# Kernel tuning notes

Measured on AMD Instinct MI355X. Metric: run time of the kernel, lower is better.

The kernel has to match this reference:

```python
import jax, jax.numpy as jnp
import numpy as np

OMEGA = 30.0
N_PTS, D_IN, HID, D_OUT, N_BLOCKS = 262144, 3, 128, 1, 7


def setup_inputs() -> dict:
    key = jax.random.key(0)
    ks = jax.random.split(key, 10)
    u = lambda k, shape, lim: jax.random.uniform(k, shape, jnp.float32, -lim, lim)
    # SIREN-style coordinates in [-1, 1]
    x = jax.random.uniform(ks[0], (N_PTS, D_IN), jnp.float32, -1.0, 1.0)
    # first SineLayer: uniform(-1/in, 1/in)
    W0 = u(ks[1], (HID, D_IN), 1.0 / D_IN)
    b0 = u(ks[2], (HID,), 1.0 / np.sqrt(D_IN))
    # hidden sine layers: uniform(-sqrt(6/in)/omega, sqrt(6/in)/omega)
    lim = np.sqrt(6.0 / HID) / OMEGA
    Wa = u(ks[3], (N_BLOCKS, HID, HID), lim)
    ba = u(ks[4], (N_BLOCKS, HID), 1.0 / np.sqrt(HID))
    Wb = u(ks[5], (N_BLOCKS, HID, HID), lim)
    bb = u(ks[6], (N_BLOCKS, HID), 1.0 / np.sqrt(HID))
    # final linear: uniform(-sqrt(6/in)/30, sqrt(6/in)/30)
    Wf = u(ks[7], (D_OUT, HID), np.sqrt(6.0 / HID) / 30.0)
    bf = u(ks[8], (D_OUT,), 1.0 / np.sqrt(HID))
    return {"x": x, "W0": W0, "b0": b0, "Wa": Wa, "ba": ba,
            "Wb": Wb, "bb": bb, "Wf": Wf, "bf": bf}


def reference(x, W0, b0, Wa, ba, Wb, bb, Wf, bf):
    # First SineLayer: sin(omega * (x W0^T + b0))   -> [N, HID]
    h = jnp.sin(OMEGA * (x @ W0.T + b0))
    nb = Wa.shape[0]
    # weight_1 = 0.5 when ave_first (ndx > 1, i.e. all blocks after the first)
    w1 = jnp.where(jnp.arange(nb) > 0, 0.5, 1.0).astype(h.dtype)
    # weight_2 = 0.5 when ave_second (last residual block)
    w2 = jnp.where(jnp.arange(nb) == nb - 1, 0.5, 1.0).astype(h.dtype)

    def block(h, xs):
        Wa_i, ba_i, Wb_i, bb_i, w1_i, w2_i = xs
        s1 = jnp.sin(OMEGA * ((w1_i * h) @ Wa_i.T + ba_i))
        s2 = jnp.sin(OMEGA * (s1 @ Wb_i.T + bb_i))
        return w2_i * (h + s2), None

    h, _ = jax.lax.scan(block, h, (Wa, ba, Wb, bb, w1, w2))
    return h @ Wf.T + bf  # [N, 1]
```

## Files before the change

kernel.cpp:

```cpp
#include <hip/hip_runtime.h>

#define NPTS 262144
#define HID  128
#define NB   7
#define NMAT 14

typedef __attribute__((ext_vector_type(8))) short bf16x8;
typedef __attribute__((ext_vector_type(4))) float f32x4;
typedef __attribute__((ext_vector_type(4))) unsigned int u32x4;

constexpr float OMEGA  = 30.0f;
constexpr float INV2PI = 0.15915494309189535f;

#define WIMG_BYTES (NMAT*32768)
#define BIAS_ELEMS (NMAT*128)
__device__ __align__(16) unsigned char g_img[WIMG_BYTES + BIAS_ELEMS*4];

__device__ __forceinline__ unsigned short f2bf(float v) {
    unsigned int u = __float_as_uint(v);
    u += 0x7fffu + ((u >> 16) & 1u);
    return (unsigned short)(u >> 16);
}

__device__ __forceinline__ float sin_rev(float r) {
    return __builtin_amdgcn_sinf(__builtin_amdgcn_fractf(r));
}

__device__ __forceinline__ unsigned int cvtpk(float lo, float hi) {
    unsigned int r;
    asm("v_cvt_pk_bf16_f32 %0, %1, %2" : "=v"(r) : "v"(lo), "v"(hi));
    return r;
}

__global__ void prep(const float* __restrict__ Wa, const float* __restrict__ ba,
                     const float* __restrict__ Wb, const float* __restrict__ bb) {
    int idx = blockIdx.x * 256 + threadIdx.x;
    const float bscale = OMEGA * INV2PI;
    const int total = NMAT * HID * HID;
    if (idx < total) {
        int mi = idx >> 14, rc = idx & 16383;
        int row = rc >> 7, col = rc & 127;
        int l = mi >> 1;
        float sc = bscale, v;
        if (mi & 1) v = Wb[l*16384 + rc];
        else { v = Wa[l*16384 + rc]; if (l > 0) sc *= 0.5f; }
        int t = col >> 4, g = (col >> 2) & 3, r = col & 3;
        int kp = ((t >> 1) << 5) | (g << 3) | ((t & 1) << 2) | r;
        int byte = mi*32768 + row*256 + ((kp*2) ^ ((row & 7) << 4));
        *(unsigned short*)(g_img + byte) = f2bf(v * sc);
    } else if (idx < total + BIAS_ELEMS) {
        int e = idx - total;
        int j = e >> 7, f = e & 127, l = j >> 1;
        float v = (j & 1) ? bb[l*HID + f] : ba[l*HID + f];
        ((float*)(g_img + WIMG_BYTES))[e] = v * bscale;
    }
}

#define LDS_BYTES 72704

__launch_bounds__(512, 2)
__global__ void siren_mlp(const float* __restrict__ x,
                          const float* __restrict__ W0,
                          const float* __restrict__ b0,
                          const float* __restrict__ Wf,
                          const float* __restrict__ bfin,
                          float* __restrict__ out) {
    extern __shared__ char smem[];
    float* bsc = (float*)(smem + 65536);

    const int tid  = threadIdx.x;
    const int lane = tid & 63;
    const int w    = tid >> 6;
    const int l16  = lane & 15;
    const int g    = lane >> 4;
    const int swz  = (l16 & 7) << 4;
    const int ptb  = blockIdx.x * 256 + w * 32;
    const float bscale = OMEGA * INV2PI;

    u32x4 st[4];
    {
        const u32x4* gp = (const u32x4*)(g_img);
        #pragma unroll
        for (int i = 0; i < 4; ++i) st[i] = gp[w*256 + i*64 + lane];
    }
    u32x4 bld;
    if (tid < 448) bld = ((const u32x4*)(g_img + WIMG_BYTES))[tid];

    f32x4 resid[2][8];
    #pragma unroll
    for (int s = 0; s < 2; ++s) {
        int pt = ptb + 16*s + l16;
        float x0 = x[3*pt], x1 = x[3*pt+1], x2 = x[3*pt+2];
        #pragma unroll
        for (int t = 0; t < 8; ++t)
            #pragma unroll
            for (int r = 0; r < 4; ++r) {
                int f = 16*t + 4*g + r;
                float arg = (x0*W0[3*f] + x1*W0[3*f+1] + x2*W0[3*f+2] + b0[f]) * bscale;
                resid[s][t][r] = sin_rev(arg);
            }
    }
    {
        u32x4* lp = (u32x4*)smem;
        #pragma unroll
        for (int i = 0; i < 4; ++i) lp[w*256 + i*64 + lane] = st[i];
        if (tid < 448) ((u32x4*)bsc)[tid] = bld;
    }
    __syncthreads();

    unsigned int bfr[2][4][4];
    f32x4 acc[2][8];

    #pragma unroll 1
    for (int blk = 0; blk < NB; ++blk) {
        #pragma unroll
        for (int s = 0; s < 2; ++s)
            #pragma unroll
            for (int t = 0; t < 8; ++t) {
                bfr[s][t>>1][(t&1)*2]   = cvtpk(resid[s][t][0], resid[s][t][1]);
                bfr[s][t>>1][(t&1)*2+1] = cvtpk(resid[s][t][2], resid[s][t][3]);
            }
        {
            const u32x4* gp = (const u32x4*)(g_img + (2*blk+1)*32768);
            #pragma unroll
            for (int i = 0; i < 4; ++i) st[i] = gp[w*256 + i*64 + lane];
        }
        {
            const float* bj = bsc + (2*blk)*128;
            #pragma unroll
            for (int t = 0; t < 8; ++t) {
                f32x4 bv = *(const f32x4*)(bj + 16*t + 4*g);
                acc[0][t] = bv; acc[1][t] = bv;
            }
            const char* wb = smem;
            #pragma unroll
            for (int ks = 0; ks < 4; ++ks) {
                u32x4 u0 = {bfr[0][ks][0], bfr[0][ks][1], bfr[0][ks][2], bfr[0][ks][3]};
                u32x4 u1 = {bfr[1][ks][0], bfr[1][ks][1], bfr[1][ks][2], bfr[1][ks][3]};
                bf16x8 bf0 = __builtin_bit_cast(bf16x8, u0);
                bf16x8 bf1 = __builtin_bit_cast(bf16x8, u1);
                #pragma unroll
                for (int t = 0; t < 8; ++t) {
                    bf16x8 a = *(const bf16x8*)(wb + (16*t + l16)*256 + ((64*ks + 16*g) ^ swz));
                    acc[0][t] = __builtin_amdgcn_mfma_f32_16x16x32_bf16(a, bf0, acc[0][t], 0,0,0);
                    acc[1][t] = __builtin_amdgcn_mfma_f32_16x16x32_bf16(a, bf1, acc[1][t], 0,0,0);
                }
            }
        }
        #pragma unroll
        for (int s = 0; s < 2; ++s)
            #pragma unroll
            for (int t = 0; t < 8; ++t) {
                float v0 = sin_rev(acc[s][t][0]);
                float v1 = sin_rev(acc[s][t][1]);
                float v2 = sin_rev(acc[s][t][2]);
                float v3 = sin_rev(acc[s][t][3]);
                bfr[s][t>>1][(t&1)*2]   = cvtpk(v0, v1);
                bfr[s][t>>1][(t&1)*2+1] = cvtpk(v2, v3);
            }
        {
            u32x4* lp = (u32x4*)(smem + 32768);
            #pragma unroll
            for (int i = 0; i < 4; ++i) lp[w*256 + i*64 + lane] = st[i];
        }
        __syncthreads();
        if (blk < NB-1) {
            const u32x4* gp = (const u32x4*)(g_img + (2*blk+2)*32768);
            #pragma unroll
            for (int i = 0; i < 4; ++i) st[i] = gp[w*256 + i*64 + lane];
        }
        {
            const float* bj = bsc + (2*blk+1)*128;
            #pragma unroll
            for (int t = 0; t < 8; ++t) {
                f32x4 bv = *(const f32x4*)(bj + 16*t + 4*g);
                acc[0][t] = bv; acc[1][t] = bv;
            }
            const char* wb = smem + 32768;
            #pragma unroll
            for (int ks = 0; ks < 4; ++ks) {
                u32x4 u0 = {bfr[0][ks][0], bfr[0][ks][1], bfr[0][ks][2], bfr[0][ks][3]};
                u32x4 u1 = {bfr[1][ks][0], bfr[1][ks][1], bfr[1][ks][2], bfr[1][ks][3]};
                bf16x8 bf0 = __builtin_bit_cast(bf16x8, u0);
                bf16x8 bf1 = __builtin_bit_cast(bf16x8, u1);
                #pragma unroll
                for (int t = 0; t < 8; ++t) {
                    bf16x8 a = *(const bf16x8*)(wb + (16*t + l16)*256 + ((64*ks + 16*g) ^ swz));
                    acc[0][t] = __builtin_amdgcn_mfma_f32_16x16x32_bf16(a, bf0, acc[0][t], 0,0,0);
                    acc[1][t] = __builtin_amdgcn_mfma_f32_16x16x32_bf16(a, bf1, acc[1][t], 0,0,0);
                }
            }
        }
        const float w2 = (blk == NB-1) ? 0.5f : 1.0f;
        #pragma unroll
        for (int s = 0; s < 2; ++s)
            #pragma unroll
            for (int t = 0; t < 8; ++t)
                #pragma unroll
                for (int r = 0; r < 4; ++r)
                    resid[s][t][r] = w2 * (resid[s][t][r] + sin_rev(acc[s][t][r]));
        if (blk < NB-1) {
            u32x4* lp = (u32x4*)smem;
            #pragma unroll
            for (int i = 0; i < 4; ++i) lp[w*256 + i*64 + lane] = st[i];
        }
        __syncthreads();
    }

    #pragma unroll
    for (int s = 0; s < 2; ++s) {
        float part = 0.f;
        #pragma unroll
        for (int t = 0; t < 8; ++t) {
            f32x4 wv = *(const f32x4*)(Wf + 16*t + 4*g);
            part += resid[s][t][0]*wv[0] + resid[s][t][1]*wv[1]
                  + resid[s][t][2]*wv[2] + resid[s][t][3]*wv[3];
        }
        part += __shfl_xor(part, 16);
        part += __shfl_xor(part, 32);
        if (g == 0) out[ptb + 16*s + l16] = part + bfin[0];
    }
}

extern "C" void kernel_launch(void* const* d_in, const int* in_sizes, int n_in,
                              void* d_out, int out_size, void* d_ws, size_t ws_size,
                              hipStream_t stream) {
    const float* x   = (const float*)d_in[0];
    const float* W0  = (const float*)d_in[1];
    const float* b0  = (const float*)d_in[2];
    const float* Wa  = (const float*)d_in[3];
    const float* ba  = (const float*)d_in[4];
    const float* Wb  = (const float*)d_in[5];
    const float* bb  = (const float*)d_in[6];
    const float* Wf  = (const float*)d_in[7];
    const float* bf_ = (const float*)d_in[8];

    prep<<<dim3(903), dim3(256), 0, stream>>>(Wa, ba, Wb, bb);
    hipFuncSetAttribute(reinterpret_cast<const void*>(siren_mlp),
                        hipFuncAttributeMaxDynamicSharedMemorySize, LDS_BYTES);
    siren_mlp<<<dim3(NPTS/256), dim3(512), LDS_BYTES, stream>>>(
        x, W0, b0, Wf, bf_, (float*)d_out);
}
```

Before: 152.8 us.

## Interleave sine activations with MFMA k-slices using dual accumulator sets

Keeps two separate accumulator sets, one per layer of the residual block, so the sine and bf16 packing of the previous layer's outputs happens slice by slice inside the next matmul's k loop. The residual update is deferred into the next block's first matmul. The final 0.5 scaling moves into the output projection. The aim is to overlap transcendental ALU work with MFMA issue instead of running them in separate phases. The block loop is now unrolled and launch bounds relaxed to one workgroup per CU, so the higher register demand may lower occupancy.

```diff
diff --git a/kernel.cpp b/kernel.cpp
--- a/kernel.cpp
+++ b/kernel.cpp
@@ -58,7 +58,7 @@
 
 #define LDS_BYTES 72704
 
-__launch_bounds__(512, 2)
+__launch_bounds__(512, 1)
 __global__ void siren_mlp(const float* __restrict__ x,
                           const float* __restrict__ W0,
                           const float* __restrict__ b0,
@@ -108,60 +108,57 @@
     }
     __syncthreads();
 
-    unsigned int bfr[2][4][4];
-    f32x4 acc[2][8];
-
-    #pragma unroll 1
+    f32x4 acc1[2][8], acc2[2][8];
+    #pragma unroll
+    for (int s = 0; s < 2; ++s)
+        #pragma unroll
+        for (int t = 0; t < 8; ++t) acc2[s][t] = (f32x4){0.f, 0.f, 0.f, 0.f};
+
     for (int blk = 0; blk < NB; ++blk) {
-        #pragma unroll
-        for (int s = 0; s < 2; ++s)
-            #pragma unroll
-            for (int t = 0; t < 8; ++t) {
-                bfr[s][t>>1][(t&1)*2]   = cvtpk(resid[s][t][0], resid[s][t][1]);
-                bfr[s][t>>1][(t&1)*2+1] = cvtpk(resid[s][t][2], resid[s][t][3]);
-            }
-        {
-            const u32x4* gp = (const u32x4*)(g_img + (2*blk+1)*32768);
-            #pragma unroll
-            for (int i = 0; i < 4; ++i) st[i] = gp[w*256 + i*64 + lane];
-        }
+        {
+            const u32x4* gq = (const u32x4*)(g_img + (2*blk+1)*32768);
+            #pragma unroll
+            for (int i = 0; i < 4; ++i) st[i] = gq[w*256 + i*64 + lane];
+        }
+
         {
             const float* bj = bsc + (2*blk)*128;
             #pragma unroll
             for (int t = 0; t < 8; ++t) {
                 f32x4 bv = *(const f32x4*)(bj + 16*t + 4*g);
-                acc[0][t] = bv; acc[1][t] = bv;
+                acc1[0][t] = bv; acc1[1][t] = bv;
             }
             const char* wb = smem;
             #pragma unroll
             for (int ks = 0; ks < 4; ++ks) {
-                u32x4 u0 = {bfr[0][ks][0], bfr[0][ks][1], bfr[0][ks][2], bfr[0][ks][3]};
-                u32x4 u1 = {bfr[1][ks][0], bfr[1][ks][1], bfr[1][ks][2], bfr[1][ks][3]};
+                unsigned int pk[2][4];
+                #pragma unroll
+                for (int s = 0; s < 2; ++s)
+                    #pragma unroll
+                    for (int tt = 0; tt < 2; ++tt) {
+                        int t = 2*ks + tt;
+                        #pragma unroll
+                        for (int r = 0; r < 4; ++r)
+                            resid[s][t][r] += sin_rev(acc2[s][t][r]);
+                        pk[s][tt*2]   = cvtpk(resid[s][t][0], resid[s][t][1]);
+                        pk[s][tt*2+1] = cvtpk(resid[s][t][2], resid[s][t][3]);
+                    }
+                u32x4 u0 = {pk[0][0], pk[0][1], pk[0][2], pk[0][3]};
+                u32x4 u1 = {pk[1][0], pk[1][1], pk[1][2], pk[1][3]};
                 bf16x8 bf0 = __builtin_bit_cast(bf16x8, u0);
                 bf16x8 bf1 = __builtin_bit_cast(bf16x8, u1);
                 #pragma unroll
                 for (int t = 0; t < 8; ++t) {
                     bf16x8 a = *(const bf16x8*)(wb + (16*t + l16)*256 + ((64*ks + 16*g) ^ swz));
-                    acc[0][t] = __builtin_amdgcn_mfma_f32_16x16x32_bf16(a, bf0, acc[0][t], 0,0,0);
-                    acc[1][t] = __builtin_amdgcn_mfma_f32_16x16x32_bf16(a, bf1, acc[1][t], 0,0,0);
+                    acc1[0][t] = __builtin_amdgcn_mfma_f32_16x16x32_bf16(a, bf0, acc1[0][t], 0,0,0);
+                    acc1[1][t] = __builtin_amdgcn_mfma_f32_16x16x32_bf16(a, bf1, acc1[1][t], 0,0,0);
                 }
             }
         }
-        #pragma unroll
-        for (int s = 0; s < 2; ++s)
-            #pragma unroll
-            for (int t = 0; t < 8; ++t) {
-                float v0 = sin_rev(acc[s][t][0]);
-                float v1 = sin_rev(acc[s][t][1]);
-                float v2 = sin_rev(acc[s][t][2]);
-                float v3 = sin_rev(acc[s][t][3]);
-                bfr[s][t>>1][(t&1)*2]   = cvtpk(v0, v1);
-                bfr[s][t>>1][(t&1)*2+1] = cvtpk(v2, v3);
-            }
-        {
-            u32x4* lp = (u32x4*)(smem + 32768);
-            #pragma unroll
-            for (int i = 0; i < 4; ++i) lp[w*256 + i*64 + lane] = st[i];
+        {
+            u32x4* lq = (u32x4*)(smem + 32768);
+            #pragma unroll
+            for (int i = 0; i < 4; ++i) lq[w*256 + i*64 + lane] = st[i];
         }
         __syncthreads();
         if (blk < NB-1) {
@@ -169,36 +166,42 @@
             #pragma unroll
             for (int i = 0; i < 4; ++i) st[i] = gp[w*256 + i*64 + lane];
         }
+
         {
             const float* bj = bsc + (2*blk+1)*128;
             #pragma unroll
             for (int t = 0; t < 8; ++t) {
                 f32x4 bv = *(const f32x4*)(bj + 16*t + 4*g);
-                acc[0][t] = bv; acc[1][t] = bv;
+                acc2[0][t] = bv; acc2[1][t] = bv;
             }
             const char* wb = smem + 32768;
             #pragma unroll
             for (int ks = 0; ks < 4; ++ks) {
-                u32x4 u0 = {bfr[0][ks][0], bfr[0][ks][1], bfr[0][ks][2], bfr[0][ks][3]};
-                u32x4 u1 = {bfr[1][ks][0], bfr[1][ks][1], bfr[1][ks][2], bfr[1][ks][3]};
+                unsigned int pk[2][4];
+                #pragma unroll
+                for (int s = 0; s < 2; ++s)
+                    #pragma unroll
+                    for (int tt = 0; tt < 2; ++tt) {
+                        int t = 2*ks + tt;
+                        float v0 = sin_rev(acc1[s][t][0]);
+                        float v1 = sin_rev(acc1[s][t][1]);
+                        float v2 = sin_rev(acc1[s][t][2]);
+                        float v3 = sin_rev(acc1[s][t][3]);
+                        pk[s][tt*2]   = cvtpk(v0, v1);
+                        pk[s][tt*2+1] = cvtpk(v2, v3);
+                    }
+                u32x4 u0 = {pk[0][0], pk[0][1], pk[0][2], pk[0][3]};
+                u32x4 u1 = {pk[1][0], pk[1][1], pk[1][2], pk[1][3]};
                 bf16x8 bf0 = __builtin_bit_cast(bf16x8, u0);
                 bf16x8 bf1 = __builtin_bit_cast(bf16x8, u1);
                 #pragma unroll
                 for (int t = 0; t < 8; ++t) {
                     bf16x8 a = *(const bf16x8*)(wb + (16*t + l16)*256 + ((64*ks + 16*g) ^ swz));
-                    acc[0][t] = __builtin_amdgcn_mfma_f32_16x16x32_bf16(a, bf0, acc[0][t], 0,0,0);
-                    acc[1][t] = __builtin_amdgcn_mfma_f32_16x16x32_bf16(a, bf1, acc[1][t], 0,0,0);
+                    acc2[0][t] = __builtin_amdgcn_mfma_f32_16x16x32_bf16(a, bf0, acc2[0][t], 0,0,0);
+                    acc2[1][t] = __builtin_amdgcn_mfma_f32_16x16x32_bf16(a, bf1, acc2[1][t], 0,0,0);
                 }
             }
         }
-        const float w2 = (blk == NB-1) ? 0.5f : 1.0f;
-        #pragma unroll
-        for (int s = 0; s < 2; ++s)
-            #pragma unroll
-            for (int t = 0; t < 8; ++t)
-                #pragma unroll
-                for (int r = 0; r < 4; ++r)
-                    resid[s][t][r] = w2 * (resid[s][t][r] + sin_rev(acc[s][t][r]));
         if (blk < NB-1) {
             u32x4* lp = (u32x4*)smem;
             #pragma unroll
@@ -213,8 +216,11 @@
         #pragma unroll
         for (int t = 0; t < 8; ++t) {
             f32x4 wv = *(const f32x4*)(Wf + 16*t + 4*g);
-            part += resid[s][t][0]*wv[0] + resid[s][t][1]*wv[1]
-                  + resid[s][t][2]*wv[2] + resid[s][t][3]*wv[3];
+            #pragma unroll
+            for (int r = 0; r < 4; ++r) {
+                float hn = 0.5f * (resid[s][t][r] + sin_rev(acc2[s][t][r]));
+                part += hn * wv[r];
+            }
         }
         part += __shfl_xor(part, 16);
         part += __shfl_xor(part, 32);
```

Measured after the change: 148.8 us. 1.03x faster.
